# Performance work log

Hardware: AMD Instinct MI355X
Metric: run time of the kernel (lower is better)

The kernel has to match this reference:

```python
import jax, jax.numpy as jnp
import numpy as np

# PaTH attention (training path, attention_mask=None):
#   score(t,s) = q_t^T (H_t H_{t-1} ... H_{s+1}) k_s,  H_i = I - beta_i w_i w_i^T (w_i unit-norm)
# computed in closed form via a UT/WY-style triangular solve, then causal softmax with
# FoX-style forget gate: logits += cumsum(logsigmoid(g))_t - cumsum(logsigmoid(g))_s.

NUM_HEADS = 32
HEAD_DIM = 64
CONV_K = 3
NEG_INF = -1e30


def _forward(hidden_states, Wq, Wk, Wv, Ww1, Ww2, conv_w, Wbt, bbt, Wg, bg, Wo):
    B, T, D = hidden_states.shape
    H, hd, Kc = NUM_HEADS, HEAD_DIM, CONV_K
    h = hidden_states
    q = h @ Wq                                   # [B,T,D]
    k = h @ Wk
    v = h @ Wv
    w = (h @ Ww1) @ Ww2                          # low-rank w_proj (rank 32)
    beta = jax.nn.sigmoid(h @ Wbt + bbt) * 2.0   # [B,T,H], in (0,2)
    g = jax.nn.log_sigmoid(h @ Wg + bg)          # [B,T,H] forget gate (log-space)
    # causal depthwise short conv (kernel 3, no bias) + silu on w
    wp = jnp.pad(w, ((0, 0), (Kc - 1, 0), (0, 0)))
    w = sum(wp[:, j:j + T, :] * conv_w[:, j] for j in range(Kc))
    w = jax.nn.silu(w)
    split = lambda x: x.reshape(B, T, H, hd)
    q, k, v, w = split(q), split(k), split(v), split(w)
    w = w * jax.lax.rsqrt(jnp.sum(w * w, axis=-1, keepdims=True))  # l2_norm per head
    # pairwise inner products, [B,H,T,S]
    Dqk = jnp.einsum('bthd,bshd->bhts', q, k)
    E = jnp.einsum('bthd,bshd->bhts', q, w)
    S = jnp.einsum('bthd,bshd->bhts', w, k)
    L = jnp.einsum('bthd,bshd->bhts', w, w)
    bcol = jnp.transpose(beta, (0, 2, 1))[:, :, None, :]  # beta_i indexed by column i
    strict = jnp.tril(jnp.ones((T, T), bool), -1)
    # C[t,s] = w_t^T (H_{t-1}...H_{s+1}) k_s solves (I + strict(L) diag(beta)) C = strict(S)
    M = jnp.eye(T, dtype=q.dtype) + jnp.where(strict, L * bcol, 0.0)
    rhs = jnp.where(strict, S, 0.0)
    C = jax.scipy.linalg.solve_triangular(M, rhs, lower=True, unit_diagonal=True)
    causal = jnp.tril(jnp.ones((T, T), bool))
    # A[t,s] = q_t^T k_s - sum_{s<i<=t} (q_t^T w_i) beta_i C[i,s]
    EB = jnp.where(causal, E, 0.0) * bcol
    A = Dqk - EB @ C
    G = jnp.cumsum(jnp.transpose(g, (0, 2, 1)), axis=-1)  # [B,H,T]
    logits = A * (hd ** -0.5) + G[..., :, None] - G[..., None, :]
    logits = jnp.where(causal, logits, NEG_INF)
    P = jax.nn.softmax(logits, axis=-1)
    o = jnp.einsum('bhts,bshd->bthd', P, v).reshape(B, T, D)
    return o @ Wo


def setup_inputs() -> dict:
    key = jax.random.key(0)
    ks = jax.random.split(key, 12)
    B, T, D, H, Kc = 1, 1024, 2048, NUM_HEADS, CONV_K
    r = lambda k, shape, scale: jax.random.normal(k, shape, dtype=jnp.float32) * scale
    s = D ** -0.5
    return {
        'hidden_states': r(ks[0], (B, T, D), 1.0),
        'Wq': r(ks[1], (D, D), s),
        'Wk': r(ks[2], (D, D), s),
        'Wv': r(ks[3], (D, D), s),
        'Ww1': r(ks[4], (D, 32), s),
        'Ww2': r(ks[5], (32, D), 32 ** -0.5),
        'conv_w': r(ks[6], (D, Kc), Kc ** -0.5),
        'Wbt': r(ks[7], (D, H), s),
        'bbt': r(ks[8], (H,), 1.0),
        'Wg': r(ks[9], (D, H), s),
        'bg': r(ks[10], (H,), 1.0),
        'Wo': r(ks[11], (D, D), s),
    }


def reference(hidden_states, Wq, Wk, Wv, Ww1, Ww2, conv_w, Wbt, bbt, Wg, bg, Wo):
    return _forward(hidden_states, Wq, Wk, Wv, Ww1, Ww2, conv_w, Wbt, bbt, Wg, bg, Wo)
```

## Files before the change

kernel.cpp:

```cpp
#include <hip/hip_runtime.h>
#include <hip/hip_bf16.h>

typedef __hip_bfloat16 bf16;
typedef unsigned short ushort_t;

#define T_  1024
#define D_  2048
#define H_  32
#define HD_ 64

static const size_t TT_ = (size_t)T_ * T_;
static const size_t TD_ = (size_t)T_ * D_;

__device__ __forceinline__ ushort_t f2bf(float v) {
    bf16 b = __float2bfloat16(v);
    return *(ushort_t*)&b;
}
__device__ __forceinline__ float bf2f(ushort_t u) {
    bf16 b = *(bf16*)&u;
    return __bfloat162float(b);
}

typedef __attribute__((ext_vector_type(8))) short frag8;
typedef __attribute__((ext_vector_type(4))) float f32x4;
typedef __attribute__((ext_vector_type(4))) unsigned short u16x4;
typedef __attribute__((ext_vector_type(8))) unsigned short u16x8;

#define MFMA16(a, b, c) __builtin_amdgcn_mfma_f32_16x16x32_bf16((a), (b), (c), 0, 0, 0)

template <int OUT>
__global__ __launch_bounds__(256) void mfma_gemm(
    const ushort_t* __restrict__ A, const ushort_t* __restrict__ Bt,
    void* __restrict__ Cout, void* __restrict__ Cout2, int M, int N, int K)
{
    __shared__ short Al[128 * 32];
    __shared__ short Bl[128 * 32];
    int tid = threadIdx.x;
    int w = tid >> 6, l = tid & 63;
    int row0 = blockIdx.y * 128, col0 = blockIdx.x * 128;
    int mq = (w >> 1) * 64, nq = (w & 1) * 64;
    int lm = l & 15, kq = l >> 4;
    f32x4 acc[4][4] = {};
    const ushort_t* Ap = A + (size_t)row0 * K;
    const ushort_t* Bp = Bt + (size_t)col0 * K;
    for (int kk = 0; kk < K; kk += 32) {
        __syncthreads();
#pragma unroll
        for (int r = 0; r < 2; r++) {
            int c = r * 256 + w * 64 + l;
            int row = c >> 2, kc = (c & 3) * 8;
            const ushort_t* ga = Ap + (size_t)row * K + kk + kc;
            const ushort_t* gb = Bp + (size_t)row * K + kk + kc;
            short* la = Al + (size_t)(r * 256 + w * 64) * 8;
            short* lb = Bl + (size_t)(r * 256 + w * 64) * 8;
            __builtin_amdgcn_global_load_lds((const __attribute__((address_space(1))) void*)ga,
                                             (__attribute__((address_space(3))) void*)la, 16, 0, 0);
            __builtin_amdgcn_global_load_lds((const __attribute__((address_space(1))) void*)gb,
                                             (__attribute__((address_space(3))) void*)lb, 16, 0, 0);
        }
        __builtin_amdgcn_s_waitcnt(0);
        __syncthreads();
        frag8 af[4], bfg[4];
#pragma unroll
        for (int i = 0; i < 4; i++)
            af[i] = *(const frag8*)&Al[(size_t)(mq + i * 16 + lm) * 32 + kq * 8];
#pragma unroll
        for (int j = 0; j < 4; j++)
            bfg[j] = *(const frag8*)&Bl[(size_t)(nq + j * 16 + lm) * 32 + kq * 8];
#pragma unroll
        for (int i = 0; i < 4; i++)
#pragma unroll
            for (int j = 0; j < 4; j++)
                acc[i][j] = MFMA16(af[i], bfg[j], acc[i][j]);
    }
#pragma unroll
    for (int i = 0; i < 4; i++)
#pragma unroll
        for (int j = 0; j < 4; j++)
#pragma unroll
            for (int r = 0; r < 4; r++) {
                int row = row0 + mq + i * 16 + kq * 4 + r;
                int col = col0 + nq + j * 16 + lm;
                float v = acc[i][j][r];
                if (OUT == 0) {
                    ((float*)Cout)[(size_t)row * N + col] = v;
                } else {
                    ushort_t* q = (ushort_t*)Cout;
                    int which = col >> 11, cl = col & 2047;
                    int hd = cl >> 6, d = cl & 63;
                    if (which == 0)
                        q[((size_t)hd * M + row) * 64 + d] = f2bf(v);
                    else if (which == 1)
                        q[(size_t)M * 2048 + ((size_t)hd * M + row) * 64 + d] = f2bf(v);
                    else if (which == 2)
                        q[(size_t)M * 4096 + ((size_t)hd * 64 + d) * M + row] = f2bf(v);
                    else
                        ((float*)Cout2)[(size_t)row * 128 + (col - 6144)] = v;
                }
            }
}

__global__ void transpose_convert(const float* __restrict__ W, ushort_t* __restrict__ Wt,
                                  int R, int Cc)
{
    __shared__ float tile[32][33];
    int bx = blockIdx.x * 32, by = blockIdx.y * 32;
    int tx = threadIdx.x, ty = threadIdx.y;
    for (int i = ty; i < 32; i += 8)
        tile[i][tx] = W[(size_t)(by + i) * Cc + bx + tx];
    __syncthreads();
    for (int i = ty; i < 32; i += 8)
        Wt[(size_t)(bx + i) * R + by + tx] = f2bf(tile[tx][i]);
}

__global__ void pack96(const float* __restrict__ Ww1, const float* __restrict__ Wbt,
                       const float* __restrict__ Wg, ushort_t* __restrict__ dst)
{
    int r = blockIdx.x;
    int k = blockIdx.y * 256 + threadIdx.x;
    float v = 0.f;
    if (r < 32)       v = Ww1[(size_t)k * 32 + r];
    else if (r < 64)  v = Wbt[(size_t)k * 32 + (r - 32)];
    else if (r < 96)  v = Wg[(size_t)k * 32 + (r - 64)];
    dst[(size_t)r * 2048 + k] = f2bf(v);
}

__global__ void convert_bf16(const float* __restrict__ in, ushort_t* __restrict__ out, int n)
{
    int i = blockIdx.x * 256 + threadIdx.x;
    if (i < n) out[i] = f2bf(in[i]);
}

__global__ void bg96(const float* __restrict__ s96, const float* __restrict__ bbt,
                     const float* __restrict__ bgp, ushort_t* __restrict__ w1bf,
                     float* __restrict__ betaB, float* __restrict__ Gb)
{
    int idx = blockIdx.x * 256 + threadIdx.x;
    int t = idx >> 7, o = idx & 127;
    if (o >= 96) return;
    float v = s96[(size_t)t * 128 + o];
    if (o < 32) {
        w1bf[(size_t)t * 32 + o] = f2bf(v);
    } else if (o < 64) {
        float xb = v + bbt[o - 32];
        betaB[(size_t)t * H_ + (o - 32)] = 2.f / (1.f + expf(-xb));
    } else {
        float xg = v + bgp[o - 64];
        Gb[(size_t)t * H_ + (o - 64)] =
            (xg >= 0.f) ? -log1pf(expf(-xg)) : (xg - log1pf(expf(xg)));
    }
}

__global__ void scan_g(float* __restrict__ G)
{
    int h = blockIdx.x;
    int tid = threadIdx.x;
    __shared__ float psum[256];
    float v[4];
    float s = 0.f;
#pragma unroll
    for (int r = 0; r < 4; r++) {
        v[r] = G[(size_t)(tid * 4 + r) * H_ + h];
        s += v[r];
    }
    psum[tid] = s;
    __syncthreads();
    for (int off = 1; off < 256; off <<= 1) {
        float t = (tid >= off) ? psum[tid - off] : 0.f;
        __syncthreads();
        psum[tid] += t;
        __syncthreads();
    }
    float run = (tid > 0) ? psum[tid - 1] : 0.f;
#pragma unroll
    for (int r = 0; r < 4; r++) {
        run += v[r];
        G[(size_t)(tid * 4 + r) * H_ + h] = run;
    }
}

__global__ void conv_silu_norm(const float* __restrict__ wr, const float* __restrict__ convw,
                               ushort_t* __restrict__ wh)
{
    int b = blockIdx.x;
    int t = b >> 5, h = b & 31;
    int d = threadIdx.x;
    int c = h * 64 + d;
    float c0 = convw[c * 3 + 0];
    float c1 = convw[c * 3 + 1];
    float c2 = convw[c * 3 + 2];
    float x = c2 * wr[(size_t)t * D_ + c];
    if (t >= 1) x += c1 * wr[(size_t)(t - 1) * D_ + c];
    if (t >= 2) x += c0 * wr[(size_t)(t - 2) * D_ + c];
    float y = x / (1.f + expf(-x));
    float ss = y * y;
    for (int off = 32; off > 0; off >>= 1) ss += __shfl_xor(ss, off, 64);
    wh[((size_t)h * T_ + t) * 64 + d] = f2bf(y * rsqrtf(ss));
}

__global__ __launch_bounds__(256) void pairdotLC(
    const ushort_t* __restrict__ kh, const ushort_t* __restrict__ wh,
    const float* __restrict__ betaB,
    ushort_t* __restrict__ ELb, ushort_t* __restrict__ Ct, int hs)
{
    int s0 = blockIdx.x * 64, t0 = blockIdx.y * 64, z = blockIdx.z;
    if (s0 > t0) return;
    int head = hs + z;
    const ushort_t* kb = kh + (size_t)head * T_ * 64;
    const ushort_t* wb = wh + (size_t)head * T_ * 64;
    ushort_t* Lz = ELb + (size_t)z * TT_;
    ushort_t* Cz = Ct + (size_t)z * TT_;
    int tid = threadIdx.x;
    int w = tid >> 6, l = tid & 63;
    int lm = l & 15, kq = l >> 4;
    int rowA = t0 + w * 16 + lm;
    f32x4 accL[4] = {}, accS[4] = {};
#pragma unroll
    for (int kk = 0; kk < 64; kk += 32) {
        frag8 aw = *(const frag8*)&wb[(size_t)rowA * 64 + kk + kq * 8];
#pragma unroll
        for (int j = 0; j < 4; j++) {
            int colr = s0 + j * 16 + lm;
            frag8 bw = *(const frag8*)&wb[(size_t)colr * 64 + kk + kq * 8];
            frag8 bk = *(const frag8*)&kb[(size_t)colr * 64 + kk + kq * 8];
            accL[j] = MFMA16(aw, bw, accL[j]);
            accS[j] = MFMA16(aw, bk, accS[j]);
        }
    }
    int m0 = w * 16 + kq * 4;
#pragma unroll
    for (int j = 0; j < 4; j++) {
        int s = s0 + j * 16 + lm;
        float beta = betaB[(size_t)s * H_ + head];
        ushort_t cl[4];
#pragma unroll
        for (int r = 0; r < 4; r++) {
            int t = t0 + m0 + r;
            Lz[(size_t)t * T_ + s] = f2bf((s < t) ? accL[j][r] * beta : 0.f);
            cl[r] = f2bf((s < t) ? accS[j][r] : 0.f);
        }
        *(u16x4*)&Cz[(size_t)s * T_ + t0 + m0] = *(u16x4*)cl;
    }
}

__global__ void diag_inv(const ushort_t* __restrict__ Lb, ushort_t* __restrict__ Minv)
{
    int bi = blockIdx.x, z = blockIdx.y;
    const ushort_t* Lh = Lb + (size_t)z * TT_;
    __shared__ float Nb[64][65];
    __shared__ float Xc[64][65];
    int tid = threadIdx.x;
    for (int i = tid; i < 4096; i += 64) {
        int r = i >> 6, c = i & 63;
        Nb[r][c] = (c < r) ? bf2f(Lh[(size_t)(bi * 64 + r) * T_ + bi * 64 + c]) : 0.f;
    }
    __syncthreads();
    int j = tid;
    for (int t = 0; t < 64; t++) {
        float v = (t == j) ? 1.f : 0.f;
        for (int i = j; i < t; i++) v -= Nb[t][i] * Xc[i][j];
        Xc[t][j] = v;
    }
    __syncthreads();
    ushort_t* Mo = Minv + ((size_t)z * 16 + bi) * 4096;
    for (int i = tid; i < 4096; i += 64) Mo[i] = f2bf(Xc[i >> 6][i & 63]);
}

__global__ __launch_bounds__(256) void solve_mfma(
    ushort_t* __restrict__ Ct, const ushort_t* __restrict__ Lb,
    const ushort_t* __restrict__ Minv)
{
    int ct = blockIdx.x, z = blockIdx.y;
    ushort_t* Cz = Ct + (size_t)z * TT_;
    const ushort_t* Lz = Lb + (size_t)z * TT_;
    __shared__ ushort_t Cl[64][136];
    __shared__ ushort_t Ll[64][136];
    __shared__ ushort_t Xbt[64][72];
    int tid = threadIdx.x;
    int w = tid >> 6, l = tid & 63;
    int lm = l & 15, kq = l >> 4;
    int s0 = ct * 64;
    int m0 = w * 16 + kq * 4;
    for (int bi = ct; bi < 16; bi++) {
        f32x4 acc[4] = {};
        for (int kkc = s0; kkc < bi * 64; kkc += 128) {
            int len = bi * 64 - kkc; if (len > 128) len = 128;
            int lsh = (len == 128) ? 4 : 3;
            __syncthreads();
            for (int i = tid; i < (64 << lsh); i += 256) {
                int r = i >> lsh, c = (i & ((1 << lsh) - 1)) * 8;
                *(u16x8*)&Cl[r][c] = *(const u16x8*)&Cz[(size_t)(s0 + r) * T_ + kkc + c];
                *(u16x8*)&Ll[r][c] = *(const u16x8*)&Lz[(size_t)(bi * 64 + r) * T_ + kkc + c];
            }
            __syncthreads();
            for (int kk2 = 0; kk2 < len; kk2 += 32) {
                frag8 a = *(const frag8*)&Ll[w * 16 + lm][kk2 + kq * 8];
#pragma unroll
                for (int j = 0; j < 4; j++) {
                    frag8 b = *(const frag8*)&Cl[j * 16 + lm][kk2 + kq * 8];
                    acc[j] = MFMA16(a, b, acc[j]);
                }
            }
        }
        __syncthreads();
#pragma unroll
        for (int j = 0; j < 4; j++) {
            int sc = s0 + j * 16 + lm;
            u16x4 rhs = *(const u16x4*)&Cz[(size_t)sc * T_ + bi * 64 + m0];
            ushort_t xb[4];
#pragma unroll
            for (int r = 0; r < 4; r++) xb[r] = f2bf(bf2f(rhs[r]) - acc[j][r]);
            *(u16x4*)&Xbt[j * 16 + lm][m0] = *(u16x4*)xb;
        }
        __syncthreads();
        f32x4 res[4] = {};
        const ushort_t* Mo = Minv + ((size_t)z * 16 + bi) * 4096;
#pragma unroll
        for (int kk = 0; kk < 64; kk += 32) {
            frag8 a = *(const frag8*)&Mo[(size_t)(w * 16 + lm) * 64 + kk + kq * 8];
#pragma unroll
            for (int j = 0; j < 4; j++) {
                frag8 b = *(const frag8*)&Xbt[j * 16 + lm][kk + kq * 8];
                res[j] = MFMA16(a, b, res[j]);
            }
        }
#pragma unroll
        for (int j = 0; j < 4; j++) {
            int sc = s0 + j * 16 + lm;
            ushort_t cr[4];
#pragma unroll
            for (int r = 0; r < 4; r++) cr[r] = f2bf(res[j][r]);
            *(u16x4*)&Cz[(size_t)sc * T_ + bi * 64 + m0] = *(u16x4*)cr;
        }
        __syncthreads();
    }
}

__global__ __launch_bounds__(256) void flash_split(
    const ushort_t* __restrict__ qh, const ushort_t* __restrict__ kh,
    const ushort_t* __restrict__ vt, const ushort_t* __restrict__ wh,
    const ushort_t* __restrict__ Ct, const float* __restrict__ betaB,
    const float* __restrict__ Gb, ushort_t* __restrict__ Op,
    float* __restrict__ ml, int hs)
{
    int st = blockIdx.x, tb = blockIdx.y, z = blockIdx.z;
    if (st > tb) return;
    int t0 = tb * 64, s0 = st * 64;
    int head = hs + z;
    const ushort_t* qb = qh + (size_t)head * T_ * 64;
    const ushort_t* kb = kh + (size_t)head * T_ * 64;
    const ushort_t* vb = vt + (size_t)head * 64 * T_;
    const ushort_t* wb = wh + (size_t)head * T_ * 64;
    const ushort_t* Cz = Ct + (size_t)z * TT_;
    __shared__ ushort_t Kl[64][72];
    __shared__ ushort_t Vl[64][72];
    __shared__ ushort_t Wl[64][72];
    __shared__ ushort_t Cl[64][72];
    __shared__ ushort_t Pl[4][16][72];
    int tid = threadIdx.x;
    int w = tid >> 6, l = tid & 63;
    int lm = l & 15, kq = l >> 4;
    int rowA = t0 + w * 16 + lm;
    int m0 = w * 16 + kq * 4;
    for (int i = tid; i < 512; i += 256) {
        int r = i >> 3, c = (i & 7) * 8;
        *(u16x8*)&Kl[r][c] = *(const u16x8*)&kb[(size_t)(s0 + r) * 64 + c];
        *(u16x8*)&Vl[r][c] = *(const u16x8*)&vb[(size_t)r * T_ + s0 + c];
    }
    frag8 aq0 = *(const frag8*)&qb[(size_t)rowA * 64 + kq * 8];
    frag8 aq1 = *(const frag8*)&qb[(size_t)rowA * 64 + 32 + kq * 8];
    __syncthreads();
    f32x4 x[4] = {};
#pragma unroll
    for (int j = 0; j < 4; j++) {
        frag8 b0 = *(const frag8*)&Kl[j * 16 + lm][kq * 8];
        frag8 b1 = *(const frag8*)&Kl[j * 16 + lm][32 + kq * 8];
        x[j] = MFMA16(aq0, b0, x[j]);
        x[j] = MFMA16(aq1, b1, x[j]);
    }
    for (int kc = s0; kc < t0 + 64; kc += 64) {
        __syncthreads();
        for (int i = tid; i < 512; i += 256) {
            int r = i >> 3, c = (i & 7) * 8;
            *(u16x8*)&Wl[r][c] = *(const u16x8*)&wb[(size_t)(kc + r) * 64 + c];
            *(u16x8*)&Cl[r][c] = *(const u16x8*)&Cz[(size_t)(s0 + r) * T_ + kc + c];
        }
        __syncthreads();
        f32x4 eq[4] = {};
#pragma unroll
        for (int jj = 0; jj < 4; jj++) {
            frag8 b0 = *(const frag8*)&Wl[jj * 16 + lm][kq * 8];
            frag8 b1 = *(const frag8*)&Wl[jj * 16 + lm][32 + kq * 8];
            eq[jj] = MFMA16(aq0, b0, eq[jj]);
            eq[jj] = MFMA16(aq1, b1, eq[jj]);
        }
#pragma unroll
        for (int jj = 0; jj < 4; jj++) {
            int k = kc + jj * 16 + lm;
            float beta = betaB[(size_t)k * H_ + head];
#pragma unroll
            for (int r = 0; r < 4; r++) {
                int t = t0 + m0 + r;
                float v = (k <= t) ? -eq[jj][r] * beta : 0.f;
                Pl[w][kq * 4 + r][jj * 16 + lm] = f2bf(v);
            }
        }
#pragma unroll
        for (int kk2 = 0; kk2 < 64; kk2 += 32) {
            frag8 a = *(const frag8*)&Pl[w][lm][kk2 + kq * 8];
#pragma unroll
            for (int j = 0; j < 4; j++) {
                frag8 b = *(const frag8*)&Cl[j * 16 + lm][kk2 + kq * 8];
                x[j] = MFMA16(a, b, x[j]);
            }
        }
    }
    float lg[4][4];
#pragma unroll
    for (int j = 0; j < 4; j++) {
        int s = s0 + j * 16 + lm;
        float g = Gb[(size_t)s * H_ + head];
#pragma unroll
        for (int r = 0; r < 4; r++) {
            int t = t0 + m0 + r;
            lg[j][r] = (s <= t) ? (x[j][r] * 0.125f - g) : -1e30f;
        }
    }
    float mrow[4];
#pragma unroll
    for (int r = 0; r < 4; r++)
        mrow[r] = fmaxf(fmaxf(lg[0][r], lg[1][r]), fmaxf(lg[2][r], lg[3][r]));
#pragma unroll
    for (int d = 1; d < 16; d <<= 1)
#pragma unroll
        for (int r = 0; r < 4; r++) mrow[r] = fmaxf(mrow[r], __shfl_xor(mrow[r], d, 64));
    float lrow[4] = {0.f, 0.f, 0.f, 0.f};
#pragma unroll
    for (int j = 0; j < 4; j++)
#pragma unroll
        for (int r = 0; r < 4; r++) {
            float p = __expf(lg[j][r] - mrow[r]);
            lg[j][r] = p;
            lrow[r] += p;
        }
#pragma unroll
    for (int d = 1; d < 16; d <<= 1)
#pragma unroll
        for (int r = 0; r < 4; r++) lrow[r] += __shfl_xor(lrow[r], d, 64);
#pragma unroll
    for (int j = 0; j < 4; j++)
#pragma unroll
        for (int r = 0; r < 4; r++)
            Pl[w][kq * 4 + r][j * 16 + lm] = f2bf(lg[j][r]);
    f32x4 o[4] = {};
#pragma unroll
    for (int j = 0; j < 4; j++) {
        frag8 b0 = *(const frag8*)&Vl[j * 16 + lm][kq * 8];
        frag8 b1 = *(const frag8*)&Vl[j * 16 + lm][32 + kq * 8];
        frag8 a0 = *(const frag8*)&Pl[w][lm][kq * 8];
        frag8 a1 = *(const frag8*)&Pl[w][lm][32 + kq * 8];
        o[j] = MFMA16(a0, b0, o[j]);
        o[j] = MFMA16(a1, b1, o[j]);
    }
    size_t pbase = (((size_t)z * 16 + tb) * 16 + st) * 4096;
#pragma unroll
    for (int j = 0; j < 4; j++)
#pragma unroll
        for (int r = 0; r < 4; r++)
            Op[pbase + (size_t)(m0 + r) * 64 + j * 16 + lm] = f2bf(o[j][r]);
    if (lm == 0) {
        size_t mbase = (((size_t)z * 16 + tb) * 16 + st) * 128;
#pragma unroll
        for (int r = 0; r < 4; r++) {
            ml[mbase + m0 + r] = mrow[r];
            ml[mbase + 64 + m0 + r] = lrow[r];
        }
    }
}

__global__ __launch_bounds__(256) void combine(
    const ushort_t* __restrict__ Op, const float* __restrict__ ml,
    ushort_t* __restrict__ of, int hs)
{
    int tb = blockIdx.x, z = blockIdx.y;
    int head = hs + z;
    int tid = threadIdx.x;
    int row = tid >> 2, cg = (tid & 3) * 16;
    size_t mb0 = (((size_t)z * 16 + tb) * 16) * 128;
    float M = -1e30f;
    for (int st = 0; st <= tb; st++)
        M = fmaxf(M, ml[mb0 + (size_t)st * 128 + row]);
    float acc[16] = {};
    float lsum = 0.f;
    for (int st = 0; st <= tb; st++) {
        float mp = ml[mb0 + (size_t)st * 128 + row];
        float lp = ml[mb0 + (size_t)st * 128 + 64 + row];
        float sc = __expf(mp - M);
        lsum += lp * sc;
        const ushort_t* op = Op + (((size_t)z * 16 + tb) * 16 + st) * 4096 + (size_t)row * 64 + cg;
#pragma unroll
        for (int i = 0; i < 16; i++) acc[i] += bf2f(op[i]) * sc;
    }
    float inv = 1.f / lsum;
    int t = tb * 64 + row;
    ushort_t* dst = of + (size_t)t * D_ + (size_t)head * 64 + cg;
#pragma unroll
    for (int i = 0; i < 16; i++) dst[i] = f2bf(acc[i] * inv);
}

extern "C" void kernel_launch(void* const* d_in, const int* in_sizes, int n_in,
                              void* d_out, int out_size, void* d_ws, size_t ws_size,
                              hipStream_t stream)
{
    const float* h     = (const float*)d_in[0];
    const float* Wq    = (const float*)d_in[1];
    const float* Wk    = (const float*)d_in[2];
    const float* Wv    = (const float*)d_in[3];
    const float* Ww1   = (const float*)d_in[4];
    const float* Ww2   = (const float*)d_in[5];
    const float* convw = (const float*)d_in[6];
    const float* Wbt   = (const float*)d_in[7];
    const float* bbt   = (const float*)d_in[8];
    const float* Wg    = (const float*)d_in[9];
    const float* bgp   = (const float*)d_in[10];
    const float* Wo    = (const float*)d_in[11];
    float* out = (float*)d_out;

    float* ws = (float*)d_ws;
    size_t off = 0;
    auto allocF = [&](size_t nf) { float* p = ws + off; off += (nf + 1023) & ~(size_t)1023; return p; };

    float*    wr    = allocF(TD_);
    float*    s96   = allocF((size_t)T_ * 128);
    float*    betaB = allocF((size_t)T_ * H_);
    float*    Gb    = allocF((size_t)T_ * H_);
    ushort_t* h_bf  = (ushort_t*)allocF(TD_ / 2);
    ushort_t* of_bf = h_bf;
    ushort_t* w1bf  = (ushort_t*)allocF((size_t)T_ * 32 / 2);
    ushort_t* Ww2t  = (ushort_t*)allocF((size_t)D_ * 32 / 2);
    ushort_t* Wtc   = (ushort_t*)allocF((size_t)6272 * D_ / 2);
    ushort_t* qkv   = (ushort_t*)allocF((size_t)3 * TD_ / 2);
    ushort_t* qh    = qkv;
    ushort_t* kh    = qkv + TD_;
    ushort_t* vt    = qkv + 2 * TD_;
    ushort_t* wh    = (ushort_t*)allocF(TD_ / 2);

    size_t fixedF = off;
    size_t capF = ws_size / 4;
    size_t perHead = TT_ + ((size_t)16 * 4096) / 2 + (size_t)16 * 16 * 128 + 2048;
    int NH = 32;
    while (NH > 1 && fixedF + (size_t)NH * perHead > capF) NH >>= 1;
    ushort_t* ELb = (ushort_t*)allocF((size_t)NH * TT_ / 2);
    ushort_t* Ct  = (ushort_t*)allocF((size_t)NH * TT_ / 2);
    ushort_t* Mv  = (ushort_t*)allocF((size_t)NH * 16 * 4096 / 2);
    float*    mlB = allocF((size_t)NH * 16 * 16 * 128);

    dim3 blk(256);
    dim3 tcvB(32, 8);
    dim3 tcvG(D_ / 32, D_ / 32);

    convert_bf16<<<dim3((TD_ + 255) / 256), blk, 0, stream>>>(h, h_bf, (int)TD_);
    transpose_convert<<<tcvG, tcvB, 0, stream>>>(Wq, Wtc, D_, D_);
    transpose_convert<<<tcvG, tcvB, 0, stream>>>(Wk, Wtc + (size_t)D_ * D_, D_, D_);
    transpose_convert<<<tcvG, tcvB, 0, stream>>>(Wv, Wtc + (size_t)2 * D_ * D_, D_, D_);
    pack96<<<dim3(128, 8), blk, 0, stream>>>(Ww1, Wbt, Wg, Wtc + (size_t)3 * D_ * D_);
    mfma_gemm<3><<<dim3(6272 / 128, T_ / 128), blk, 0, stream>>>(
        h_bf, Wtc, qkv, s96, T_, 6272, D_);

    bg96<<<dim3(T_ * 128 / 256), blk, 0, stream>>>(s96, bbt, bgp, w1bf, betaB, Gb);
    scan_g<<<dim3(H_), blk, 0, stream>>>(Gb);
    transpose_convert<<<dim3(D_ / 32, 1), tcvB, 0, stream>>>(Ww2, Ww2t, 32, D_);
    mfma_gemm<0><<<dim3(D_ / 128, T_ / 128), blk, 0, stream>>>(
        w1bf, Ww2t, wr, nullptr, T_, D_, 32);
    conv_silu_norm<<<dim3(T_ * H_), dim3(64), 0, stream>>>(wr, convw, wh);

    int nChunks = H_ / NH;
    for (int c = 0; c < nChunks; c++) {
        int hs = c * NH;
        pairdotLC<<<dim3(16, 16, NH), blk, 0, stream>>>(kh, wh, betaB, ELb, Ct, hs);
        diag_inv<<<dim3(16, NH), dim3(64), 0, stream>>>(ELb, Mv);
        solve_mfma<<<dim3(16, NH), blk, 0, stream>>>(Ct, ELb, Mv);
        flash_split<<<dim3(16, 16, NH), blk, 0, stream>>>(
            qh, kh, vt, wh, Ct, betaB, Gb, ELb, mlB, hs);
        combine<<<dim3(16, NH), blk, 0, stream>>>(ELb, mlB, of_bf, hs);
    }

    transpose_convert<<<tcvG, tcvB, 0, stream>>>(Wo, Wtc, D_, D_);
    mfma_gemm<0><<<dim3(D_ / 128, T_ / 128), blk, 0, stream>>>(
        of_bf, Wtc, out, nullptr, T_, D_, D_);
}
```

Baseline: 900.3 us.

## Precompute beta-scaled E matrix once instead of recomputing per flash tile

A new kernel computes the masked, beta-scaled q·w inner products (E) once per head and stores them as a bf16 TxT matrix, reusing the ELb buffer after the solve. flash_split now loads E tiles from global memory instead of recomputing q·w with MFMA for every (s-tile, k-chunk) pair, which removes redundant recomputation across the split s-tiles. The split outputs move to a new OpB buffer, so per-head workspace grows and fewer heads may fit per chunk, and each flash block now reads an extra TxT stream from memory.

```diff
diff --git a/kernel.cpp b/kernel.cpp
--- a/kernel.cpp
+++ b/kernel.cpp
@@ -243,6 +243,43 @@
     }
 }
 
+__global__ __launch_bounds__(256) void pairdotE(
+    const ushort_t* __restrict__ qh, const ushort_t* __restrict__ wh,
+    const float* __restrict__ betaB, ushort_t* __restrict__ ELb, int hs)
+{
+    int s0 = blockIdx.x * 64, t0 = blockIdx.y * 64, z = blockIdx.z;
+    if (s0 > t0) return;
+    int head = hs + z;
+    const ushort_t* qb = qh + (size_t)head * T_ * 64;
+    const ushort_t* wb = wh + (size_t)head * T_ * 64;
+    ushort_t* Ez = ELb + (size_t)z * TT_;
+    int tid = threadIdx.x;
+    int w = tid >> 6, l = tid & 63;
+    int lm = l & 15, kq = l >> 4;
+    int rowA = t0 + w * 16 + lm;
+    f32x4 accE[4] = {};
+#pragma unroll
+    for (int kk = 0; kk < 64; kk += 32) {
+        frag8 aq = *(const frag8*)&qb[(size_t)rowA * 64 + kk + kq * 8];
+#pragma unroll
+        for (int j = 0; j < 4; j++) {
+            frag8 bw = *(const frag8*)&wb[(size_t)(s0 + j * 16 + lm) * 64 + kk + kq * 8];
+            accE[j] = MFMA16(aq, bw, accE[j]);
+        }
+    }
+    int m0 = w * 16 + kq * 4;
+#pragma unroll
+    for (int j = 0; j < 4; j++) {
+        int s = s0 + j * 16 + lm;
+        float beta = betaB[(size_t)s * H_ + head];
+#pragma unroll
+        for (int r = 0; r < 4; r++) {
+            int t = t0 + m0 + r;
+            Ez[(size_t)t * T_ + s] = f2bf((s <= t) ? -accE[j][r] * beta : 0.f);
+        }
+    }
+}
+
 __global__ void diag_inv(const ushort_t* __restrict__ Lb, ushort_t* __restrict__ Minv)
 {
     int bi = blockIdx.x, z = blockIdx.y;
@@ -338,10 +375,9 @@
 
 __global__ __launch_bounds__(256) void flash_split(
     const ushort_t* __restrict__ qh, const ushort_t* __restrict__ kh,
-    const ushort_t* __restrict__ vt, const ushort_t* __restrict__ wh,
-    const ushort_t* __restrict__ Ct, const float* __restrict__ betaB,
-    const float* __restrict__ Gb, ushort_t* __restrict__ Op,
-    float* __restrict__ ml, int hs)
+    const ushort_t* __restrict__ vt, const ushort_t* __restrict__ Em,
+    const ushort_t* __restrict__ Ct, const float* __restrict__ Gb,
+    ushort_t* __restrict__ Op, float* __restrict__ ml, int hs)
 {
     int st = blockIdx.x, tb = blockIdx.y, z = blockIdx.z;
     if (st > tb) return;
@@ -350,13 +386,13 @@
     const ushort_t* qb = qh + (size_t)head * T_ * 64;
     const ushort_t* kb = kh + (size_t)head * T_ * 64;
     const ushort_t* vb = vt + (size_t)head * 64 * T_;
-    const ushort_t* wb = wh + (size_t)head * T_ * 64;
+    const ushort_t* Ez = Em + (size_t)z * TT_;
     const ushort_t* Cz = Ct + (size_t)z * TT_;
     __shared__ ushort_t Kl[64][72];
     __shared__ ushort_t Vl[64][72];
-    __shared__ ushort_t Wl[64][72];
+    __shared__ ushort_t El[64][72];
     __shared__ ushort_t Cl[64][72];
-    __shared__ ushort_t Pl[4][16][72];
+    __shared__ ushort_t Pl[4][16][76];
     int tid = threadIdx.x;
     int w = tid >> 6, l = tid & 63;
     int lm = l & 15, kq = l >> 4;
@@ -382,32 +418,13 @@
         __syncthreads();
         for (int i = tid; i < 512; i += 256) {
             int r = i >> 3, c = (i & 7) * 8;
-            *(u16x8*)&Wl[r][c] = *(const u16x8*)&wb[(size_t)(kc + r) * 64 + c];
+            *(u16x8*)&El[r][c] = *(const u16x8*)&Ez[(size_t)(t0 + r) * T_ + kc + c];
             *(u16x8*)&Cl[r][c] = *(const u16x8*)&Cz[(size_t)(s0 + r) * T_ + kc + c];
         }
         __syncthreads();
-        f32x4 eq[4] = {};
-#pragma unroll
-        for (int jj = 0; jj < 4; jj++) {
-            frag8 b0 = *(const frag8*)&Wl[jj * 16 + lm][kq * 8];
-            frag8 b1 = *(const frag8*)&Wl[jj * 16 + lm][32 + kq * 8];
-            eq[jj] = MFMA16(aq0, b0, eq[jj]);
-            eq[jj] = MFMA16(aq1, b1, eq[jj]);
-        }
-#pragma unroll
-        for (int jj = 0; jj < 4; jj++) {
-            int k = kc + jj * 16 + lm;
-            float beta = betaB[(size_t)k * H_ + head];
-#pragma unroll
-            for (int r = 0; r < 4; r++) {
-                int t = t0 + m0 + r;
-                float v = (k <= t) ? -eq[jj][r] * beta : 0.f;
-                Pl[w][kq * 4 + r][jj * 16 + lm] = f2bf(v);
-            }
-        }
 #pragma unroll
         for (int kk2 = 0; kk2 < 64; kk2 += 32) {
-            frag8 a = *(const frag8*)&Pl[w][lm][kk2 + kq * 8];
+            frag8 a = *(const frag8*)&El[w * 16 + lm][kk2 + kq * 8];
 #pragma unroll
             for (int j = 0; j < 4; j++) {
                 frag8 b = *(const frag8*)&Cl[j * 16 + lm][kk2 + kq * 8];
@@ -547,11 +564,12 @@
 
     size_t fixedF = off;
     size_t capF = ws_size / 4;
-    size_t perHead = TT_ + ((size_t)16 * 4096) / 2 + (size_t)16 * 16 * 128 + 2048;
+    size_t perHead = 3 * (TT_ / 2) + ((size_t)16 * 4096) / 2 + (size_t)16 * 16 * 128 + 3072;
     int NH = 32;
     while (NH > 1 && fixedF + (size_t)NH * perHead > capF) NH >>= 1;
     ushort_t* ELb = (ushort_t*)allocF((size_t)NH * TT_ / 2);
     ushort_t* Ct  = (ushort_t*)allocF((size_t)NH * TT_ / 2);
+    ushort_t* OpB = (ushort_t*)allocF((size_t)NH * TT_ / 2);
     ushort_t* Mv  = (ushort_t*)allocF((size_t)NH * 16 * 4096 / 2);
     float*    mlB = allocF((size_t)NH * 16 * 16 * 128);
 
@@ -580,9 +598,10 @@
         pairdotLC<<<dim3(16, 16, NH), blk, 0, stream>>>(kh, wh, betaB, ELb, Ct, hs);
         diag_inv<<<dim3(16, NH), dim3(64), 0, stream>>>(ELb, Mv);
         solve_mfma<<<dim3(16, NH), blk, 0, stream>>>(Ct, ELb, Mv);
+        pairdotE<<<dim3(16, 16, NH), blk, 0, stream>>>(qh, wh, betaB, ELb, hs);
         flash_split<<<dim3(16, 16, NH), blk, 0, stream>>>(
-            qh, kh, vt, wh, Ct, betaB, Gb, ELb, mlB, hs);
-        combine<<<dim3(16, NH), blk, 0, stream>>>(ELb, mlB, of_bf, hs);
+            qh, kh, vt, ELb, Ct, Gb, OpB, mlB, hs);
+        combine<<<dim3(16, NH), blk, 0, stream>>>(OpB, mlB, of_bf, hs);
     }
 
     transpose_convert<<<tcvG, tcvB, 0, stream>>>(Wo, Wtc, D_, D_);
```

After: 882.9 us. No clear change (-1.9%).
